# Kernel tuning notes

Measured on AMD Instinct MI355X. Metric: run time of the kernel, lower is better.

## Reference

```python
import jax, jax.numpy as jnp
import numpy as np

B = 1024
P = 8
D = 2048
NUM_IDS = 64
MARGIN = 0.3
EPS = 1e-12


def setup_inputs() -> dict:
    key = jax.random.key(0)
    k1, k2, k3 = jax.random.split(key, 3)
    feats = jax.random.normal(k1, (B, P * D), dtype=jnp.float32)
    labels = jax.random.randint(k2, (B,), 0, NUM_IDS, dtype=jnp.int64)
    subs = jax.random.randint(k3, (B,), 0, 2, dtype=jnp.int64)
    return {"feats": feats, "labels": labels, "subs": subs}


def reference(feats, labels, subs):
    b = feats.shape[0]
    f = feats.reshape(b, -1, D)  # [B, P, D]
    dt = f.dtype

    # Per-sample class centers via a single segment-mean pass
    # (equivalent to the original per-sample boolean-mask mean loop).
    seg_sum = jax.ops.segment_sum(f, labels, num_segments=NUM_IDS)  # [NUM_IDS, P, D]
    counts = jax.ops.segment_sum(jnp.ones((b,), dt), labels, num_segments=NUM_IDS)
    centers_by_id = seg_sum / jnp.maximum(counts, 1.0)[:, None, None]
    centers = centers_by_id[labels]  # [B, P, D]

    # dist_ap[i] = sum_p ||f[i,p] - center[i,p]||
    d_ap = jnp.sqrt(jnp.clip(jnp.sum((f - centers) ** 2, axis=-1), EPS, None)).sum(-1)  # [B]
    dist_ap = d_ap[:, None] + d_ap[None, :]  # [B, B]

    # pairwise_distance: dist_aa[i,j] = sum_p ||f[i,p] - f[j,p]||, via gemm trick
    sq = jnp.sum(f * f, axis=-1)  # [B, P]
    inner = jnp.einsum('ipd,jpd->ijp', f, f)  # [B, B, P]
    d2 = sq[:, None, :] + sq[None, :, :] - 2.0 * inner
    dist_aa = jnp.sqrt(jnp.clip(d2, EPS, None)).sum(-1)  # [B, B]

    # masked margin loss over negative (different-label) pairs
    mask = labels[:, None] != labels[None, :]  # [B, B] bool
    vals = jnp.clip(dist_ap - dist_aa + MARGIN, 0.0, None)
    maskf = mask.astype(dt)
    loss = jnp.sum(vals * maskf) / jnp.sum(maskf)
    return loss
```

## Files before the change

kernel.cpp:

```cpp
#include <hip/hip_runtime.h>
#include <hip/hip_bf16.h>

#define B_ 1024
#define P_ 8
#define D_ 2048
#define FD_ (P_ * D_)
#define NID 64
#define MARGIN_ 0.3f
#define EPS_ 1e-12f
#define NJOBS (136 * 8)

typedef unsigned short u16;
typedef float float4_t __attribute__((ext_vector_type(4)));

#define AS1 __attribute__((address_space(1)))
#define AS3 __attribute__((address_space(3)))

__device__ __forceinline__ float bf2f(u16 v) {
    unsigned x = (unsigned)v << 16;
    float f;
    __builtin_memcpy(&f, &x, 4);
    return f;
}

static const size_t OFF_COUNTS = 0;
static const size_t OFF_OFFS   = 256;
static const size_t OFF_PERM   = 512;
static const size_t OFF_NEG    = 4608;
static const size_t OFF_DONE   = 4616;
static const size_t OFF_POS    = 8176;
static const size_t OFF_S      = 8192;
static const size_t OFF_SQ     = 40960;
static const size_t OFF_DAP    = 73728;
static const size_t OFF_FB     = 131072;
static const size_t OFF_PD     = OFF_FB + (size_t)B_ * FD_;

__global__ void k_prep(const float* __restrict__ feats, const int* __restrict__ labels,
                       unsigned char* __restrict__ fb, float* __restrict__ sq,
                       float* countsf, int* offs, int* perm, float* negcnt,
                       float* S, float* possum, int* done) {
    int tid = threadIdx.x;
    if (blockIdx.x < B_) {
        int i = blockIdx.x;
        int w = tid >> 6, lane = tid & 63;
        const float* frow = feats + (size_t)i * FD_;
        unsigned char* brow = fb + (size_t)i * FD_;
#pragma unroll
        for (int pp = 0; pp < 2; pp++) {
            int p = w * 2 + pp;
            int off = p * D_;
            float s2 = 0.f;
#pragma unroll
            for (int ch = 0; ch < 8; ch++) {
                int d = off + ch * 256 + lane * 4;
                float4 f = *(const float4*)(frow + d);
                int pk = __builtin_amdgcn_cvt_pk_fp8_f32(f.x, f.y, 0, false);
                pk = __builtin_amdgcn_cvt_pk_fp8_f32(f.z, f.w, pk, true);
                *(unsigned int*)(brow + d) = (unsigned int)pk;
                s2 += f.x * f.x + f.y * f.y + f.z * f.z + f.w * f.w;
            }
            for (int o = 32; o; o >>= 1) s2 += __shfl_down(s2, o, 64);
            if (lane == 0) sq[i * P_ + p] = s2;
        }
        return;
    }
    __shared__ int h[NID], o[NID], cur[NID];
    if (tid < NID) h[tid] = 0;
    __syncthreads();
    for (int i = tid; i < B_; i += 256) atomicAdd(&h[labels[i]], 1);
    __syncthreads();
    if (tid == 0) {
        int acc = 0;
        long long ss = 0;
        for (int c = 0; c < NID; c++) {
            o[c] = acc;
            acc += h[c];
            ss += (long long)h[c] * h[c];
        }
        *negcnt = (float)((long long)B_ * B_ - ss);
        *possum = 0.f;
        done[0] = 0;
    }
    __syncthreads();
    if (tid < NID) {
        countsf[tid] = (float)h[tid];
        offs[tid] = o[tid];
        cur[tid] = o[tid];
    }
    __syncthreads();
    for (int i = tid; i < B_; i += 256) {
        int pos = atomicAdd(&cur[labels[i]], 1);
        perm[pos] = i;
    }
    for (int i = tid; i < B_ * P_; i += 256) S[i] = 0.f;
}

__global__ __launch_bounds__(256, 4) void k_pairs(const unsigned char* __restrict__ fb,
                                                  const float* __restrict__ sq,
                                                  const int* __restrict__ labels,
                                                  float* __restrict__ S,
                                                  u16* __restrict__ pd) {
    int t = blockIdx.x >> 3;
    const int p = blockIdx.x & 7;
    int ti = 0;
    while (t >= 16 - ti) { t -= 16 - ti; ti++; }
    const int tj = ti + t;
    const int i0 = ti * 64, j0 = tj * 64;
    const bool offdiag = (tj > ti);

    __shared__ __align__(16) unsigned char smem[16384];
    __shared__ float sqAs[64], sqBs[64];
    __shared__ int labA[64], labB[64];
    const int tid = threadIdx.x;
    const int lane = tid & 63, w = tid >> 6;
    const int wr = w >> 1, wc = w & 1;
    if (tid < 64) {
        sqAs[tid] = sq[(i0 + tid) * 8 + p];
        labA[tid] = labels[i0 + tid];
    } else if (tid < 128) {
        int u = tid - 64;
        sqBs[u] = sq[(j0 + u) * 8 + p];
        labB[u] = labels[j0 + u];
    }

    const int lhi = lane >> 4, llo = lane & 15;
    const int sl = llo & 7;
    const int lr = lane >> 3;
    const int lc = (lane & 7) ^ lr;

    unsigned char* const As = smem;
    unsigned char* const Bs = smem + 8192;

    const size_t colbase = (size_t)p * D_ + (size_t)lc * 16;
    const unsigned char* gA[2];
    const unsigned char* gB[2];
    unsigned char* lA[2];
    unsigned char* lB[2];
#pragma unroll
    for (int inst = 0; inst < 2; inst++) {
        int r0 = w * 16 + inst * 8;
        gA[inst] = fb + (size_t)(i0 + r0 + lr) * FD_ + colbase;
        gB[inst] = fb + (size_t)(j0 + r0 + lr) * FD_ + colbase;
        lA[inst] = As + r0 * 128;
        lB[inst] = Bs + r0 * 128;
    }

    float4_t acc[2][2];
#pragma unroll
    for (int a = 0; a < 2; a++)
#pragma unroll
        for (int b = 0; b < 2; b++) acc[a][b] = (float4_t){0.f, 0.f, 0.f, 0.f};

    for (int kb = 0; kb < 16; kb++) {
        const int koff = kb * 128;
        __syncthreads();
#pragma unroll
        for (int inst = 0; inst < 2; inst++) {
            __builtin_amdgcn_global_load_lds((const AS1 void*)(gA[inst] + koff),
                                             (AS3 void*)lA[inst], 16, 0, 0);
            __builtin_amdgcn_global_load_lds((const AS1 void*)(gB[inst] + koff),
                                             (AS3 void*)lB[inst], 16, 0, 0);
        }
        __syncthreads();
#pragma unroll
        for (int ks = 0; ks < 4; ks++) {
            const int pcb = ((2 * ks + (lhi >> 1)) ^ sl) * 16 + (lhi & 1) * 8;
            long af[2], bf[2];
#pragma unroll
            for (int a = 0; a < 2; a++) {
                af[a] = *(const long*)(As + (wr * 32 + a * 16 + llo) * 128 + pcb);
                bf[a] = *(const long*)(Bs + (wc * 32 + a * 16 + llo) * 128 + pcb);
            }
#pragma unroll
            for (int a = 0; a < 2; a++)
#pragma unroll
                for (int b = 0; b < 2; b++)
                    acc[a][b] = __builtin_amdgcn_mfma_f32_16x16x32_fp8_fp8(
                        af[a], bf[b], acc[a][b], 0, 0, 0);
        }
    }

    u16* outp = pd + (size_t)p * B_ * B_;
    float rs[2][4];
    float cs[2];
#pragma unroll
    for (int a = 0; a < 2; a++)
#pragma unroll
        for (int r = 0; r < 4; r++) rs[a][r] = 0.f;
#pragma unroll
    for (int b = 0; b < 2; b++) cs[b] = 0.f;
#pragma unroll
    for (int a = 0; a < 2; a++) {
        int la0 = labA[wr * 32 + a * 16 + lhi * 4 + 0];
        int la1 = labA[wr * 32 + a * 16 + lhi * 4 + 1];
        int la2 = labA[wr * 32 + a * 16 + lhi * 4 + 2];
        int la3 = labA[wr * 32 + a * 16 + lhi * 4 + 3];
#pragma unroll
        for (int b = 0; b < 2; b++) {
            int jl = wc * 32 + b * 16 + llo;
            int lb = labB[jl];
#pragma unroll
            for (int r = 0; r < 4; r++) {
                int il = wr * 32 + a * 16 + lhi * 4 + r;
                float tt = acc[a][b][r];
                float d2 = sqAs[il] + sqBs[jl] - 2.0f * tt;
                u16 bv = __bfloat16_as_ushort(__float2bfloat16(sqrtf(fmaxf(d2, EPS_))));
                outp[(size_t)(i0 + il) * B_ + (j0 + jl)] = bv;
                if (offdiag) outp[(size_t)(j0 + jl) * B_ + (i0 + il)] = bv;
                int la = (r == 0) ? la0 : (r == 1) ? la1 : (r == 2) ? la2 : la3;
                if (lb == la) {
                    rs[a][r] += tt;
                    if (offdiag) cs[b] += tt;
                }
            }
        }
    }
#pragma unroll
    for (int a = 0; a < 2; a++)
#pragma unroll
        for (int r = 0; r < 4; r++) {
            float v = rs[a][r];
            v += __shfl_xor(v, 1, 64);
            v += __shfl_xor(v, 2, 64);
            v += __shfl_xor(v, 4, 64);
            v += __shfl_xor(v, 8, 64);
            if (llo == 0)
                atomicAdd(&S[(size_t)(i0 + wr * 32 + a * 16 + lhi * 4 + r) * 8 + p], v);
        }
    if (offdiag) {
#pragma unroll
        for (int b = 0; b < 2; b++) {
            float v = cs[b];
            v += __shfl_xor(v, 16, 64);
            v += __shfl_xor(v, 32, 64);
            if (lhi == 0)
                atomicAdd(&S[(size_t)(j0 + wc * 32 + b * 16 + llo) * 8 + p], v);
        }
    }
}

__global__ void k_dap(const float* __restrict__ S, const float* __restrict__ sq,
                      const float* __restrict__ countsf, const int* __restrict__ offs,
                      const int* __restrict__ perm, float* __restrict__ dap) {
    int c = blockIdx.x;
    int tid = threadIdx.x;
    int cnt = (int)countsf[c];
    int off = offs[c];
    __shared__ float T[8];
    if (tid < 8) {
        float t = 0.f;
        for (int m = 0; m < cnt; m++) t += S[(size_t)perm[off + m] * 8 + tid];
        T[tid] = t;
    }
    __syncthreads();
    float n = fmaxf((float)cnt, 1.f);
    float inv = 1.f / n, inv2 = inv * inv;
    for (int m = tid; m < cnt; m += 64) {
        int i = perm[off + m];
        float d = 0.f;
#pragma unroll
        for (int p = 0; p < 8; p++) {
            float d2 = sq[i * 8 + p] - 2.f * inv * S[(size_t)i * 8 + p] + inv2 * T[p];
            d += sqrtf(fmaxf(d2, EPS_));
        }
        dap[i] = d;
    }
}

__global__ void k_lossred(const u16* __restrict__ pd, const float* __restrict__ dap,
                          const int* __restrict__ labels, float* possum,
                          const float* __restrict__ negcnt, int* __restrict__ done,
                          float* __restrict__ out) {
    int i = blockIdx.x;
    int tid = threadIdx.x;
    float di = dap[i];
    int li = labels[i];
    int j0 = tid * 4;
    float d0 = 0.f, d1 = 0.f, d2 = 0.f, d3 = 0.f;
#pragma unroll
    for (int p = 0; p < P_; p++) {
        ushort4 v = *(const ushort4*)&pd[(size_t)p * B_ * B_ + (size_t)i * B_ + j0];
        d0 += bf2f(v.x);
        d1 += bf2f(v.y);
        d2 += bf2f(v.z);
        d3 += bf2f(v.w);
    }
    int4 lj = *(const int4*)&labels[j0];
    float4 dj = *(const float4*)&dap[j0];
    float lsum = 0.f;
    if (lj.x != li) lsum += fmaxf(di + dj.x - d0 + MARGIN_, 0.f);
    if (lj.y != li) lsum += fmaxf(di + dj.y - d1 + MARGIN_, 0.f);
    if (lj.z != li) lsum += fmaxf(di + dj.z - d2 + MARGIN_, 0.f);
    if (lj.w != li) lsum += fmaxf(di + dj.w - d3 + MARGIN_, 0.f);
    for (int o = 32; o; o >>= 1) lsum += __shfl_down(lsum, o, 64);
    __shared__ float red[4];
    int wid = tid >> 6, lane = tid & 63;
    if (lane == 0) red[wid] = lsum;
    __syncthreads();
    if (tid == 0) {
        atomicAdd(possum, red[0] + red[1] + red[2] + red[3]);
        __threadfence();
        int v = atomicAdd(done, 1);
        if (v == B_ - 1) {
            float ps = atomicAdd(possum, 0.f);
            out[0] = ps / negcnt[0];
        }
    }
}

extern "C" void kernel_launch(void* const* d_in, const int* in_sizes, int n_in,
                              void* d_out, int out_size, void* d_ws, size_t ws_size,
                              hipStream_t stream) {
    const float* feats = (const float*)d_in[0];
    const int* labels  = (const int*)d_in[1];
    float* out = (float*)d_out;

    char* w = (char*)d_ws;
    float* countsf = (float*)(w + OFF_COUNTS);
    int* offs      = (int*)(w + OFF_OFFS);
    int* perm      = (int*)(w + OFF_PERM);
    float* negcnt  = (float*)(w + OFF_NEG);
    int* done      = (int*)(w + OFF_DONE);
    float* possum  = (float*)(w + OFF_POS);
    float* S       = (float*)(w + OFF_S);
    float* sq      = (float*)(w + OFF_SQ);
    float* dap     = (float*)(w + OFF_DAP);
    unsigned char* fb = (unsigned char*)(w + OFF_FB);
    u16* pd        = (u16*)(w + OFF_PD);

    k_prep<<<B_ + 1, 256, 0, stream>>>(feats, labels, fb, sq, countsf, offs, perm,
                                       negcnt, S, possum, done);
    k_pairs<<<NJOBS, 256, 0, stream>>>(fb, sq, labels, S, pd);
    k_dap<<<NID, 64, 0, stream>>>(S, sq, countsf, offs, perm, dap);
    k_lossred<<<B_, 256, 0, stream>>>(pd, dap, labels, possum, negcnt, done, out);
}
```

Before: 177.6 us.

## Compute each 64x64 pair tile with one wave and double-buffered LDS

The k_pairs kernel now uses a single 64-lane wave per 64x64 tile instead of four waves. Each wave holds a 4x4 grid of MFMA accumulators and stages K-blocks into a double-buffered 32KB LDS region, synchronising with explicit waitcnt instead of __syncthreads. The goal is to drop block-level barriers and overlap global-to-LDS loads with MFMA work. In exchange there are fewer waves per tile to hide latency, more registers per lane, and twice the LDS per block, which may lower occupancy.

```diff
diff --git a/kernel.cpp b/kernel.cpp
--- a/kernel.cpp
+++ b/kernel.cpp
@@ -95,11 +95,11 @@
     for (int i = tid; i < B_ * P_; i += 256) S[i] = 0.f;
 }
 
-__global__ __launch_bounds__(256, 4) void k_pairs(const unsigned char* __restrict__ fb,
-                                                  const float* __restrict__ sq,
-                                                  const int* __restrict__ labels,
-                                                  float* __restrict__ S,
-                                                  u16* __restrict__ pd) {
+__global__ __launch_bounds__(64, 2) void k_pairs(const unsigned char* __restrict__ fb,
+                                                 const float* __restrict__ sq,
+                                                 const int* __restrict__ labels,
+                                                 float* __restrict__ S,
+                                                 u16* __restrict__ pd) {
     int t = blockIdx.x >> 3;
     const int p = blockIdx.x & 7;
     int ti = 0;
@@ -108,100 +108,97 @@
     const int i0 = ti * 64, j0 = tj * 64;
     const bool offdiag = (tj > ti);
 
-    __shared__ __align__(16) unsigned char smem[16384];
+    __shared__ __align__(16) unsigned char smem[32768];
     __shared__ float sqAs[64], sqBs[64];
     __shared__ int labA[64], labB[64];
-    const int tid = threadIdx.x;
-    const int lane = tid & 63, w = tid >> 6;
-    const int wr = w >> 1, wc = w & 1;
-    if (tid < 64) {
-        sqAs[tid] = sq[(i0 + tid) * 8 + p];
-        labA[tid] = labels[i0 + tid];
-    } else if (tid < 128) {
-        int u = tid - 64;
-        sqBs[u] = sq[(j0 + u) * 8 + p];
-        labB[u] = labels[j0 + u];
-    }
+    const int lane = threadIdx.x;
+
+    sqAs[lane] = sq[(i0 + lane) * 8 + p];
+    labA[lane] = labels[i0 + lane];
+    sqBs[lane] = sq[(j0 + lane) * 8 + p];
+    labB[lane] = labels[j0 + lane];
 
     const int lhi = lane >> 4, llo = lane & 15;
     const int sl = llo & 7;
     const int lr = lane >> 3;
     const int lc = (lane & 7) ^ lr;
 
-    unsigned char* const As = smem;
-    unsigned char* const Bs = smem + 8192;
-
-    const size_t colbase = (size_t)p * D_ + (size_t)lc * 16;
-    const unsigned char* gA[2];
-    const unsigned char* gB[2];
-    unsigned char* lA[2];
-    unsigned char* lB[2];
-#pragma unroll
-    for (int inst = 0; inst < 2; inst++) {
-        int r0 = w * 16 + inst * 8;
-        gA[inst] = fb + (size_t)(i0 + r0 + lr) * FD_ + colbase;
-        gB[inst] = fb + (size_t)(j0 + r0 + lr) * FD_ + colbase;
-        lA[inst] = As + r0 * 128;
-        lB[inst] = Bs + r0 * 128;
-    }
-
-    float4_t acc[2][2];
-#pragma unroll
-    for (int a = 0; a < 2; a++)
-#pragma unroll
-        for (int b = 0; b < 2; b++) acc[a][b] = (float4_t){0.f, 0.f, 0.f, 0.f};
-
-    for (int kb = 0; kb < 16; kb++) {
-        const int koff = kb * 128;
-        __syncthreads();
-#pragma unroll
-        for (int inst = 0; inst < 2; inst++) {
-            __builtin_amdgcn_global_load_lds((const AS1 void*)(gA[inst] + koff),
-                                             (AS3 void*)lA[inst], 16, 0, 0);
-            __builtin_amdgcn_global_load_lds((const AS1 void*)(gB[inst] + koff),
-                                             (AS3 void*)lB[inst], 16, 0, 0);
-        }
-        __syncthreads();
-#pragma unroll
-        for (int ks = 0; ks < 4; ks++) {
-            const int pcb = ((2 * ks + (lhi >> 1)) ^ sl) * 16 + (lhi & 1) * 8;
-            long af[2], bf[2];
-#pragma unroll
-            for (int a = 0; a < 2; a++) {
-                af[a] = *(const long*)(As + (wr * 32 + a * 16 + llo) * 128 + pcb);
-                bf[a] = *(const long*)(Bs + (wc * 32 + a * 16 + llo) * 128 + pcb);
-            }
-#pragma unroll
-            for (int a = 0; a < 2; a++)
-#pragma unroll
-                for (int b = 0; b < 2; b++)
-                    acc[a][b] = __builtin_amdgcn_mfma_f32_16x16x32_fp8_fp8(
-                        af[a], bf[b], acc[a][b], 0, 0, 0);
-        }
-    }
+    const unsigned char* baseA = fb + (size_t)(i0 + lr) * FD_ + (size_t)p * D_ + (size_t)lc * 16;
+    const unsigned char* baseB = fb + (size_t)(j0 + lr) * FD_ + (size_t)p * D_ + (size_t)lc * 16;
+
+    float4_t acc[4][4];
+#pragma unroll
+    for (int a = 0; a < 4; a++)
+#pragma unroll
+        for (int b = 0; b < 4; b++) acc[a][b] = (float4_t){0.f, 0.f, 0.f, 0.f};
+
+#define STAGE(BUF, KB)                                                                  \
+    {                                                                                   \
+        asm volatile("s_waitcnt lgkmcnt(0)" ::: "memory");  \
+        _Pragma("unroll") for (int inst = 0; inst < 8; inst++) {                        \
+            __builtin_amdgcn_global_load_lds(                                           \
+                (const AS1 void*)(baseA + inst * (8 * FD_) + (KB) * 128),               \
+                (AS3 void*)(smem + (BUF) * 16384 + inst * 1024), 16, 0, 0);             \
+            __builtin_amdgcn_global_load_lds(                                           \
+                (const AS1 void*)(baseB + inst * (8 * FD_) + (KB) * 128),               \
+                (AS3 void*)(smem + (BUF) * 16384 + 8192 + inst * 1024), 16, 0, 0);      \
+        }                                                                               \
+    }
+
+#define COMPUTE(BUF, VM)                                                                \
+    {                                                                                   \
+        asm volatile("s_waitcnt vmcnt(" VM ")" ::: "memory");  \
+        _Pragma("unroll") for (int ks = 0; ks < 4; ks++) {                              \
+            const int pcb = ((2 * ks + (lhi >> 1)) ^ sl) * 16 + (lhi & 1) * 8;          \
+            long af[4], bf[4];                                                          \
+            _Pragma("unroll") for (int a = 0; a < 4; a++)                               \
+                af[a] = *(const long*)(smem + (BUF) * 16384 + (a * 16 + llo) * 128 + pcb); \
+            _Pragma("unroll") for (int b = 0; b < 4; b++)                               \
+                bf[b] = *(const long*)(smem + (BUF) * 16384 + 8192 + (b * 16 + llo) * 128 + pcb); \
+            _Pragma("unroll") for (int a = 0; a < 4; a++)                               \
+                _Pragma("unroll") for (int b = 0; b < 4; b++)                           \
+                    acc[a][b] = __builtin_amdgcn_mfma_f32_16x16x32_fp8_fp8(             \
+                        af[a], bf[b], acc[a][b], 0, 0, 0);                              \
+        }                                                                               \
+    }
+
+    STAGE(0, 0);
+#pragma unroll 1
+    for (int kb2 = 0; kb2 < 7; kb2++) {
+        STAGE(1, 2 * kb2 + 1);
+        COMPUTE(0, "16");
+        STAGE(0, 2 * kb2 + 2);
+        COMPUTE(1, "16");
+    }
+    STAGE(1, 15);
+    COMPUTE(0, "16");
+    COMPUTE(1, "0");
+
+#undef STAGE
+#undef COMPUTE
 
     u16* outp = pd + (size_t)p * B_ * B_;
-    float rs[2][4];
-    float cs[2];
-#pragma unroll
-    for (int a = 0; a < 2; a++)
+    float rs[4][4];
+    float cs[4];
+#pragma unroll
+    for (int a = 0; a < 4; a++)
 #pragma unroll
         for (int r = 0; r < 4; r++) rs[a][r] = 0.f;
 #pragma unroll
-    for (int b = 0; b < 2; b++) cs[b] = 0.f;
-#pragma unroll
-    for (int a = 0; a < 2; a++) {
-        int la0 = labA[wr * 32 + a * 16 + lhi * 4 + 0];
-        int la1 = labA[wr * 32 + a * 16 + lhi * 4 + 1];
-        int la2 = labA[wr * 32 + a * 16 + lhi * 4 + 2];
-        int la3 = labA[wr * 32 + a * 16 + lhi * 4 + 3];
-#pragma unroll
-        for (int b = 0; b < 2; b++) {
-            int jl = wc * 32 + b * 16 + llo;
+    for (int b = 0; b < 4; b++) cs[b] = 0.f;
+#pragma unroll
+    for (int a = 0; a < 4; a++) {
+        int la0 = labA[a * 16 + lhi * 4 + 0];
+        int la1 = labA[a * 16 + lhi * 4 + 1];
+        int la2 = labA[a * 16 + lhi * 4 + 2];
+        int la3 = labA[a * 16 + lhi * 4 + 3];
+#pragma unroll
+        for (int b = 0; b < 4; b++) {
+            int jl = b * 16 + llo;
             int lb = labB[jl];
 #pragma unroll
             for (int r = 0; r < 4; r++) {
-                int il = wr * 32 + a * 16 + lhi * 4 + r;
+                int il = a * 16 + lhi * 4 + r;
                 float tt = acc[a][b][r];
                 float d2 = sqAs[il] + sqBs[jl] - 2.0f * tt;
                 u16 bv = __bfloat16_as_ushort(__float2bfloat16(sqrtf(fmaxf(d2, EPS_))));
@@ -216,7 +213,7 @@
         }
     }
 #pragma unroll
-    for (int a = 0; a < 2; a++)
+    for (int a = 0; a < 4; a++)
 #pragma unroll
         for (int r = 0; r < 4; r++) {
             float v = rs[a][r];
@@ -225,16 +222,16 @@
             v += __shfl_xor(v, 4, 64);
             v += __shfl_xor(v, 8, 64);
             if (llo == 0)
-                atomicAdd(&S[(size_t)(i0 + wr * 32 + a * 16 + lhi * 4 + r) * 8 + p], v);
+                atomicAdd(&S[(size_t)(i0 + a * 16 + lhi * 4 + r) * 8 + p], v);
         }
     if (offdiag) {
 #pragma unroll
-        for (int b = 0; b < 2; b++) {
+        for (int b = 0; b < 4; b++) {
             float v = cs[b];
             v += __shfl_xor(v, 16, 64);
             v += __shfl_xor(v, 32, 64);
             if (lhi == 0)
-                atomicAdd(&S[(size_t)(j0 + wc * 32 + b * 16 + llo) * 8 + p], v);
+                atomicAdd(&S[(size_t)(j0 + b * 16 + llo) * 8 + p], v);
         }
     }
 }
@@ -330,7 +327,7 @@
 
     k_prep<<<B_ + 1, 256, 0, stream>>>(feats, labels, fb, sq, countsf, offs, perm,
                                        negcnt, S, possum, done);
-    k_pairs<<<NJOBS, 256, 0, stream>>>(fb, sq, labels, S, pd);
+    k_pairs<<<NJOBS, 64, 0, stream>>>(fb, sq, labels, S, pd);
     k_dap<<<NID, 64, 0, stream>>>(S, sq, countsf, offs, perm, dap);
     k_lossred<<<B_, 256, 0, stream>>>(pd, dap, labels, possum, negcnt, done, out);
 }
```

After: 183.4 us. 3.3% more time.
